# Kernel optimization log

Hardware: AMD Instinct MI355X
Metric: run time of the kernel (lower is better)

## Reference

```python
import jax, jax.numpy as jnp
import numpy as np

N_NODES = 50000
N_EDGES = 800000
D_FEAT = 128
HIDDEN = 256
N_CLASSES = 2


def setup_inputs() -> dict:
    key = jax.random.key(0)
    ks = jax.random.split(key, 9)
    x = jax.random.normal(ks[0], (N_NODES, D_FEAT), dtype=jnp.float32)
    edge_index = jax.random.randint(ks[1], (2, N_EDGES), 0, N_NODES, dtype=jnp.int32)
    # SAGEConv params: lin_l (applied to aggregated neighbors), lin_r (root), bias
    s1 = 1.0 / np.sqrt(D_FEAT)
    s2 = 1.0 / np.sqrt(HIDDEN)
    W1l = jax.random.normal(ks[2], (D_FEAT, HIDDEN), dtype=jnp.float32) * s1
    W1r = jax.random.normal(ks[3], (D_FEAT, HIDDEN), dtype=jnp.float32) * s1
    b1 = jax.random.normal(ks[4], (HIDDEN,), dtype=jnp.float32) * s1
    W2l = jax.random.normal(ks[5], (HIDDEN, N_CLASSES), dtype=jnp.float32) * s2
    W2r = jax.random.normal(ks[6], (HIDDEN, N_CLASSES), dtype=jnp.float32) * s2
    b2 = jax.random.normal(ks[7], (N_CLASSES,), dtype=jnp.float32) * s2
    return {"x": x, "edge_index": edge_index, "W1l": W1l, "W1r": W1r,
            "b1": b1, "W2l": W2l, "W2r": W2r, "b2": b2}


def _sage_conv(x, src, dst, Wl, Wr, b):
    # mean-aggregate neighbor features x[src] into destination nodes
    n = x.shape[0]
    agg = jax.ops.segment_sum(x[src], dst, num_segments=n)  # [N, d]
    deg = jax.ops.segment_sum(jnp.ones((src.shape[0],), x.dtype), dst,
                              num_segments=n)
    mean = agg / jnp.maximum(deg, 1.0)[:, None]
    return mean @ Wl + x @ Wr + b


def reference(x, edge_index, W1l, W1r, b1, W2l, W2r, b2):
    src, dst = edge_index[0], edge_index[1]
    h = jax.nn.relu(_sage_conv(x, src, dst, W1l, W1r, b1))
    embeddings = h  # dropout is identity in eval mode
    out = jax.nn.sigmoid(_sage_conv(embeddings, src, dst, W2l, W2r, b2))
    return out, embeddings
```

## Files before the change

kernel.cpp:

```cpp
#include <hip/hip_runtime.h>
#include <math.h>

#define N_NODES 50000
#define N_EDGES 800000
#define D_FEAT 128
#define HIDDEN 256
#define NB_SCAN 196
#define GEMM_BLOCKS 1563

#define PREP_CVT_B 512
#define PREP_WF_B 64
#define AGG_B 2048

#define NSLICE 64
#define SLICE_E 12500
#define NPART 8
#define PART_N 6250

typedef __bf16 bf16x8 __attribute__((ext_vector_type(8)));
typedef float f32x4 __attribute__((ext_vector_type(4)));

__device__ __forceinline__ unsigned f2b(float f) {
    unsigned u = __builtin_bit_cast(unsigned, f);
    return (u + 0x7fff + ((u >> 16) & 1)) >> 16;
}

__global__ __launch_bounds__(256) void prep(
    const float* __restrict__ x,
    const float* __restrict__ W1l, const float* __restrict__ W1r,
    unsigned* __restrict__ xb, unsigned short* __restrict__ Wfrag) {
    int b = blockIdx.x;
    int t = threadIdx.x;
    if (b < PREP_CVT_B) {
        for (int g = b * 256 + t; g < 800000; g += PREP_CVT_B * 256) {
            float4 v0 = *(const float4*)(x + (size_t)g * 8);
            float4 v1 = *(const float4*)(x + (size_t)g * 8 + 4);
            uint4 o;
            o.x = f2b(v0.x) | (f2b(v0.y) << 16);
            o.y = f2b(v0.z) | (f2b(v0.w) << 16);
            o.z = f2b(v1.x) | (f2b(v1.y) << 16);
            o.w = f2b(v1.z) | (f2b(v1.w) << 16);
            int d = g >> 4;
            int j = (g & 15) << 2;
            *(uint4*)(xb + (size_t)d * 64 + j) = o;
        }
    } else {
        for (int tt = (b - PREP_CVT_B) * 256 + t; tt < 65536; tt += PREP_WF_B * 256) {
            int j = tt & 7;
            int lane = (tt >> 3) & 63;
            int ks = (tt >> 9) & 7;
            int nt = tt >> 12;
            int k = ks * 32 + ((lane >> 4) << 3) + j;
            int n = (nt << 4) + (lane & 15);
            float v = (k < 128) ? W1l[k * 256 + n] : W1r[(k - 128) * 256 + n];
            Wfrag[tt] = (unsigned short)f2b(v);
        }
    }
}

__global__ __launch_bounds__(256) void hist_kernel(const int* __restrict__ dst,
                                                   unsigned* __restrict__ arr) {
    __shared__ unsigned hist[25000];
    int i = blockIdx.x;
    int t = threadIdx.x;
    for (int k = t; k < 25000; k += 256) hist[k] = 0;
    __syncthreads();
    int e0 = i * SLICE_E;
    for (int k = t; k < SLICE_E; k += 256) {
        int d = dst[e0 + k];
        atomicAdd(&hist[d >> 1], (d & 1) ? 65536u : 1u);
    }
    __syncthreads();
    for (int d = t; d < N_NODES; d += 256)
        arr[(size_t)i * N_NODES + d] = (hist[d >> 1] >> ((d & 1) << 4)) & 0xffffu;
}

__global__ void scan1(const unsigned* __restrict__ arr, int* __restrict__ cnt,
                      int* __restrict__ bsum) {
    __shared__ int tmp[256];
    int t = threadIdx.x;
    int i = blockIdx.x * 256 + t;
    int c = 0;
    if (i < N_NODES) {
        for (int k = 0; k < NSLICE; k++) c += (int)arr[(size_t)k * N_NODES + i];
        cnt[i] = c;
    }
    tmp[t] = c;
    __syncthreads();
    for (int off = 128; off > 0; off >>= 1) {
        if (t < off) tmp[t] += tmp[t + off];
        __syncthreads();
    }
    if (t == 0) bsum[blockIdx.x] = tmp[0];
}

__global__ void scanB(const int* __restrict__ cnt, const int* __restrict__ bsum,
                      int* __restrict__ rowbeg) {
    __shared__ int bs[256];
    __shared__ int tmp[256];
    int t = threadIdx.x;
    int b = blockIdx.x;
    bs[t] = (t < NB_SCAN) ? bsum[t] : 0;
    __syncthreads();
    for (int off = 1; off < 256; off <<= 1) {
        int y = (t >= off) ? bs[t - off] : 0;
        __syncthreads();
        bs[t] += y;
        __syncthreads();
    }
    int boff = (b == 0) ? 0 : bs[b - 1];
    int i = b * 256 + t;
    int v = (i < N_NODES) ? cnt[i] : 0;
    tmp[t] = v;
    __syncthreads();
    for (int off = 1; off < 256; off <<= 1) {
        int y = (t >= off) ? tmp[t - off] : 0;
        __syncthreads();
        tmp[t] += y;
        __syncthreads();
    }
    if (i < N_NODES) rowbeg[i] = tmp[t] - v + boff;
}

__global__ __launch_bounds__(256) void offs_kernel(const int* __restrict__ rowbeg,
                                                   unsigned* __restrict__ arr) {
    int d = blockIdx.x * 256 + threadIdx.x;
    if (d >= N_NODES) return;
    unsigned running = (unsigned)rowbeg[d];
#pragma unroll 4
    for (int k = 0; k < NSLICE; k++) {
        unsigned old = arr[(size_t)k * N_NODES + d];
        arr[(size_t)k * N_NODES + d] = running;
        running += old;
    }
}

__global__ __launch_bounds__(256) void scatter_kernel(
    const int* __restrict__ src, const int* __restrict__ dst,
    const unsigned* __restrict__ arr, unsigned short* __restrict__ esrc) {
    __shared__ unsigned off[PART_N];
    int g = blockIdx.x & 7;
    int i = blockIdx.x >> 3;
    int t = threadIdx.x;
    int lo = g * PART_N;
    for (int k = t; k < PART_N; k += 256)
        off[k] = arr[(size_t)i * N_NODES + lo + k];
    __syncthreads();
    int e0 = i * SLICE_E;
    for (int k = t; k < SLICE_E; k += 256) {
        int e = e0 + k;
        int d = dst[e];
        unsigned dl = (unsigned)(d - lo);
        if (dl < (unsigned)PART_N) {
            unsigned pos = atomicAdd(&off[dl], 1u);
            esrc[pos] = (unsigned short)src[e];
        }
    }
}

__global__ __launch_bounds__(256) void agg1(
    const unsigned* __restrict__ xb, unsigned* __restrict__ mb,
    const unsigned short* __restrict__ esrc,
    const int* __restrict__ rowbeg, const int* __restrict__ cnt) {
    int wid = (blockIdx.x * 256 + threadIdx.x) >> 6;
    int lane = threadIdx.x & 63;
    for (int d = wid; d < N_NODES; d += AGG_B * 4) {
        int beg = rowbeg[d];
        int c = cnt[d];
        int end = beg + c;
        float a0 = 0.0f, a1 = 0.0f;
        for (int base = beg; base < end; base += 64) {
            int m = end - base; if (m > 64) m = 64;
            int idx = base + lane;
            int e = (int)esrc[idx < end ? idx : end - 1];
            for (int j0 = 0; j0 < m; j0 += 8) {
#pragma unroll
                for (int j = 0; j < 8; j++) {
                    int ss = __shfl(e, j0 + j);
                    unsigned u = xb[(size_t)ss * 64 + lane];
                    float sc = (j0 + j < m) ? 1.0f : 0.0f;
                    a0 += sc * __builtin_bit_cast(float, u << 16);
                    a1 += sc * __builtin_bit_cast(float, u & 0xffff0000u);
                }
            }
        }
        float inv = 1.0f / fmaxf((float)c, 1.0f);
        mb[(size_t)d * 64 + lane] = f2b(a0 * inv) | (f2b(a1 * inv) << 16);
    }
}

__global__ __launch_bounds__(256) void gemm1ps(
    const unsigned* __restrict__ mb, const unsigned* __restrict__ xb,
    const unsigned short* __restrict__ Wfrag, const float* __restrict__ b1,
    const float* __restrict__ W2l, const float* __restrict__ W2r,
    const float* __restrict__ b2,
    float* __restrict__ h, float* __restrict__ p, float* __restrict__ s) {
    __shared__ unsigned A[32 * 128];
    __shared__ float ppart[32][4];

    int r0 = blockIdx.x * 32;
    int tid = threadIdx.x;
    int w = tid >> 6;
    int lane = tid & 63;
    int quad = lane >> 4;
    int l15 = lane & 15;

    if (tid < 128) ((float*)ppart)[tid] = 0.0f;

    int sr = tid >> 3;
    int c0 = tid & 7;
#pragma unroll
    for (int j = 0; j < 4; j++) {
        int c = c0 + (j << 3);
        uint4 v;
        if (c < 16) v = *(const uint4*)(mb + (size_t)(r0 + sr) * 64 + (c << 2));
        else        v = *(const uint4*)(xb + (size_t)(r0 + sr) * 64 + ((c - 16) << 2));
        int cp = c ^ (sr & 7);
        *(uint4*)(A + sr * 128 + (cp << 2)) = v;
    }
    __syncthreads();

    f32x4 acc[8];
#pragma unroll
    for (int i = 0; i < 8; i++) acc[i] = (f32x4){0.0f, 0.0f, 0.0f, 0.0f};

    for (int ks = 0; ks < 8; ks++) {
        bf16x8 bfr[4];
#pragma unroll
        for (int nt = 0; nt < 4; nt++) {
            int ntg = (w << 2) + nt;
            uint4 raw = *(const uint4*)(Wfrag + ((((ntg << 3) + ks) << 6) + lane) * 8);
            bfr[nt] = __builtin_bit_cast(bf16x8, raw);
        }
#pragma unroll
        for (int mt = 0; mt < 2; mt++) {
            int row = (mt << 4) + l15;
            int c = (ks << 2) + quad;
            uint4 araw = *(const uint4*)(A + row * 128 + ((c ^ (row & 7)) << 2));
            bf16x8 afr = __builtin_bit_cast(bf16x8, araw);
#pragma unroll
            for (int nt = 0; nt < 4; nt++) {
                acc[(mt << 2) + nt] = __builtin_amdgcn_mfma_f32_16x16x32_bf16(
                    afr, bfr[nt], acc[(mt << 2) + nt], 0, 0, 0);
            }
        }
    }

    float w2[4][4];
#pragma unroll
    for (int nt = 0; nt < 4; nt++) {
        int col = (w << 6) + (nt << 4) + l15;
        float2 l2 = *(const float2*)(W2l + col * 2);
        float2 r2 = *(const float2*)(W2r + col * 2);
        w2[nt][0] = l2.x; w2[nt][1] = l2.y; w2[nt][2] = r2.x; w2[nt][3] = r2.y;
    }

#pragma unroll
    for (int mt = 0; mt < 2; mt++) {
        float red[4][4];
#pragma unroll
        for (int v = 0; v < 4; v++)
#pragma unroll
            for (int r = 0; r < 4; r++) red[v][r] = 0.0f;

#pragma unroll
        for (int nt = 0; nt < 4; nt++) {
            int col = (w << 6) + (nt << 4) + l15;
            float b = b1[col];
            f32x4 v = acc[(mt << 2) + nt];
#pragma unroll
            for (int r = 0; r < 4; r++) {
                float hv = v[r] + b;
                hv = hv > 0.0f ? hv : 0.0f;
                int row = r0 + (mt << 4) + (quad << 2) + r;
                if (row < N_NODES)
                    __builtin_nontemporal_store(hv, &h[(size_t)row * 256 + col]);
                red[0][r] += hv * w2[nt][0];
                red[1][r] += hv * w2[nt][1];
                red[2][r] += hv * w2[nt][2];
                red[3][r] += hv * w2[nt][3];
            }
        }
#pragma unroll
        for (int v = 0; v < 4; v++)
#pragma unroll
            for (int r = 0; r < 4; r++) {
                red[v][r] += __shfl_xor(red[v][r], 1);
                red[v][r] += __shfl_xor(red[v][r], 2);
                red[v][r] += __shfl_xor(red[v][r], 4);
                red[v][r] += __shfl_xor(red[v][r], 8);
            }
        if (l15 == 0) {
            int lrow = (mt << 4) + (quad << 2);
#pragma unroll
            for (int r = 0; r < 4; r++)
#pragma unroll
                for (int v = 0; v < 4; v++)
                    atomicAdd(&ppart[lrow + r][v], red[v][r]);
        }
    }
    __syncthreads();

    if (tid < 32) {
        int row = r0 + tid;
        if (row < N_NODES) {
            float2 pv = {ppart[tid][0], ppart[tid][1]};
            float2 sv = {ppart[tid][2] + b2[0], ppart[tid][3] + b2[1]};
            *(float2*)(p + (size_t)row * 2) = pv;
            *(float2*)(s + (size_t)row * 2) = sv;
        }
    }
}

__global__ __launch_bounds__(256) void agg2(
    const float* __restrict__ p, const float* __restrict__ s,
    const unsigned short* __restrict__ esrc,
    const int* __restrict__ rowbeg, const int* __restrict__ cnt,
    float* __restrict__ out) {
    int wid = (blockIdx.x * 256 + threadIdx.x) >> 6;
    int lane = threadIdx.x & 63;
    for (int d = wid; d < N_NODES; d += AGG_B * 4) {
        int beg = rowbeg[d];
        int c = cnt[d];
        int end = beg + c;
        float a0 = 0.0f, a1 = 0.0f;
        for (int base = beg; base < end; base += 64) {
            int idx = base + lane;
            if (idx < end) {
                int ss = (int)esrc[idx];
                float2 v = *(const float2*)(p + (size_t)ss * 2);
                a0 += v.x; a1 += v.y;
            }
        }
#pragma unroll
        for (int off = 32; off > 0; off >>= 1) {
            a0 += __shfl_down(a0, off);
            a1 += __shfl_down(a1, off);
        }
        if (lane == 0) {
            float inv = 1.0f / fmaxf((float)c, 1.0f);
            float z0 = a0 * inv + s[(size_t)d * 2 + 0];
            float z1 = a1 * inv + s[(size_t)d * 2 + 1];
            float2 o = {1.0f / (1.0f + expf(-z0)), 1.0f / (1.0f + expf(-z1))};
            *(float2*)(out + (size_t)d * 2) = o;
        }
    }
}

extern "C" void kernel_launch(void* const* d_in, const int* in_sizes, int n_in,
                              void* d_out, int out_size, void* d_ws, size_t ws_size,
                              hipStream_t stream) {
    const float* x   = (const float*)d_in[0];
    const int*   ei  = (const int*)d_in[1];
    const float* W1l = (const float*)d_in[2];
    const float* W1r = (const float*)d_in[3];
    const float* b1  = (const float*)d_in[4];
    const float* W2l = (const float*)d_in[5];
    const float* W2r = (const float*)d_in[6];
    const float* b2  = (const float*)d_in[7];

    const int* src = ei;
    const int* dst = ei + N_EDGES;

    float* out = (float*)d_out;
    float* emb = out + (size_t)N_NODES * 2;

    int* cnt    = (int*)d_ws;
    int* rowbeg = cnt + N_NODES;
    int* bsum   = rowbeg + N_NODES;
    unsigned short* esrc = (unsigned short*)(bsum + 256);
    unsigned* xb = (unsigned*)(esrc + 800064);
    unsigned* mb = xb + (size_t)50048 * 64;
    unsigned* arr = mb;
    unsigned short* Wfrag = (unsigned short*)(mb + (size_t)50048 * 64);
    float* p = (float*)(Wfrag + 65536);
    float* s = p + (size_t)N_NODES * 2;

    prep<<<PREP_CVT_B + PREP_WF_B, 256, 0, stream>>>(x, W1l, W1r, xb, Wfrag);

    hist_kernel<<<NSLICE, 256, 0, stream>>>(dst, arr);
    scan1<<<NB_SCAN, 256, 0, stream>>>(arr, cnt, bsum);
    scanB<<<NB_SCAN, 256, 0, stream>>>(cnt, bsum, rowbeg);
    offs_kernel<<<NB_SCAN, 256, 0, stream>>>(rowbeg, arr);
    scatter_kernel<<<NSLICE * NPART, 256, 0, stream>>>(src, dst, arr, esrc);

    agg1<<<AGG_B, 256, 0, stream>>>(xb, mb, esrc, rowbeg, cnt);

    gemm1ps<<<GEMM_BLOCKS, 256, 0, stream>>>(mb, xb, Wfrag, b1, W2l, W2r, b2,
                                             emb, p, s);

    agg2<<<AGG_B, 256, 0, stream>>>(p, s, esrc, rowbeg, cnt, out);
}
```

Baseline: 239.2 us.

## Vectorize agg1 gathers with 16-byte loads, fuse offs into scanB, widen hist blocks

The first-layer aggregation now has each wavefront process four neighbor rows at once. Each group of 16 lanes loads a full 256-byte bf16 row with uint4 loads, and the groups are reduced with cross-lane xor shuffles before a vectorized store. This replaces one 4-byte load per lane per neighbor. The per-slice offset computation is folded into scanB, which removes one kernel launch. The histogram kernel also uses 1024-thread blocks to speed up the LDS clear and the atomics. The cost is more registers per lane and an extra shuffle reduction in agg1.

Measured after the change: 226.4 us. 5.4% less time.

```diff
diff --git a/kernel.cpp b/kernel.cpp
--- a/kernel.cpp
+++ b/kernel.cpp
@@ -58,20 +58,20 @@
     }
 }
 
-__global__ __launch_bounds__(256) void hist_kernel(const int* __restrict__ dst,
-                                                   unsigned* __restrict__ arr) {
+__global__ __launch_bounds__(1024) void hist_kernel(const int* __restrict__ dst,
+                                                    unsigned* __restrict__ arr) {
     __shared__ unsigned hist[25000];
     int i = blockIdx.x;
     int t = threadIdx.x;
-    for (int k = t; k < 25000; k += 256) hist[k] = 0;
+    for (int k = t; k < 25000; k += 1024) hist[k] = 0;
     __syncthreads();
     int e0 = i * SLICE_E;
-    for (int k = t; k < SLICE_E; k += 256) {
+    for (int k = t; k < SLICE_E; k += 1024) {
         int d = dst[e0 + k];
         atomicAdd(&hist[d >> 1], (d & 1) ? 65536u : 1u);
     }
     __syncthreads();
-    for (int d = t; d < N_NODES; d += 256)
+    for (int d = t; d < N_NODES; d += 1024)
         arr[(size_t)i * N_NODES + d] = (hist[d >> 1] >> ((d & 1) << 4)) & 0xffffu;
 }
 
@@ -95,7 +95,7 @@
 }
 
 __global__ void scanB(const int* __restrict__ cnt, const int* __restrict__ bsum,
-                      int* __restrict__ rowbeg) {
+                      int* __restrict__ rowbeg, unsigned* __restrict__ arr) {
     __shared__ int bs[256];
     __shared__ int tmp[256];
     int t = threadIdx.x;
@@ -119,19 +119,15 @@
         tmp[t] += y;
         __syncthreads();
     }
-    if (i < N_NODES) rowbeg[i] = tmp[t] - v + boff;
-}
-
-__global__ __launch_bounds__(256) void offs_kernel(const int* __restrict__ rowbeg,
-                                                   unsigned* __restrict__ arr) {
-    int d = blockIdx.x * 256 + threadIdx.x;
-    if (d >= N_NODES) return;
-    unsigned running = (unsigned)rowbeg[d];
+    if (i < N_NODES) {
+        unsigned running = (unsigned)(tmp[t] - v + boff);
+        rowbeg[i] = (int)running;
 #pragma unroll 4
-    for (int k = 0; k < NSLICE; k++) {
-        unsigned old = arr[(size_t)k * N_NODES + d];
-        arr[(size_t)k * N_NODES + d] = running;
-        running += old;
+        for (int k = 0; k < NSLICE; k++) {
+            unsigned old = arr[(size_t)k * N_NODES + i];
+            arr[(size_t)k * N_NODES + i] = running;
+            running += old;
+        }
     }
 }
 
@@ -164,28 +160,48 @@
     const int* __restrict__ rowbeg, const int* __restrict__ cnt) {
     int wid = (blockIdx.x * 256 + threadIdx.x) >> 6;
     int lane = threadIdx.x & 63;
+    int g = lane >> 4;
+    int i = lane & 15;
     for (int d = wid; d < N_NODES; d += AGG_B * 4) {
         int beg = rowbeg[d];
         int c = cnt[d];
         int end = beg + c;
-        float a0 = 0.0f, a1 = 0.0f;
+        float acc[8];
+#pragma unroll
+        for (int f = 0; f < 8; f++) acc[f] = 0.0f;
+
         for (int base = beg; base < end; base += 64) {
             int m = end - base; if (m > 64) m = 64;
             int idx = base + lane;
             int e = (int)esrc[idx < end ? idx : end - 1];
-            for (int j0 = 0; j0 < m; j0 += 8) {
-#pragma unroll
-                for (int j = 0; j < 8; j++) {
-                    int ss = __shfl(e, j0 + j);
-                    unsigned u = xb[(size_t)ss * 64 + lane];
-                    float sc = (j0 + j < m) ? 1.0f : 0.0f;
-                    a0 += sc * __builtin_bit_cast(float, u << 16);
-                    a1 += sc * __builtin_bit_cast(float, u & 0xffff0000u);
-                }
+            for (int j0 = 0; j0 < m; j0 += 4) {
+                int ss = __shfl(e, j0 + g);
+                float sc = (j0 + g < m) ? 1.0f : 0.0f;
+                uint4 u = *(const uint4*)(xb + (size_t)ss * 64 + (i << 2));
+                acc[0] += sc * __builtin_bit_cast(float, u.x << 16);
+                acc[1] += sc * __builtin_bit_cast(float, u.x & 0xffff0000u);
+                acc[2] += sc * __builtin_bit_cast(float, u.y << 16);
+                acc[3] += sc * __builtin_bit_cast(float, u.y & 0xffff0000u);
+                acc[4] += sc * __builtin_bit_cast(float, u.z << 16);
+                acc[5] += sc * __builtin_bit_cast(float, u.z & 0xffff0000u);
+                acc[6] += sc * __builtin_bit_cast(float, u.w << 16);
+                acc[7] += sc * __builtin_bit_cast(float, u.w & 0xffff0000u);
             }
         }
-        float inv = 1.0f / fmaxf((float)c, 1.0f);
-        mb[(size_t)d * 64 + lane] = f2b(a0 * inv) | (f2b(a1 * inv) << 16);
+#pragma unroll
+        for (int f = 0; f < 8; f++) {
+            acc[f] += __shfl_xor(acc[f], 16);
+            acc[f] += __shfl_xor(acc[f], 32);
+        }
+        if (lane < 16) {
+            float inv = 1.0f / fmaxf((float)c, 1.0f);
+            uint4 o;
+            o.x = f2b(acc[0] * inv) | (f2b(acc[1] * inv) << 16);
+            o.y = f2b(acc[2] * inv) | (f2b(acc[3] * inv) << 16);
+            o.z = f2b(acc[4] * inv) | (f2b(acc[5] * inv) << 16);
+            o.w = f2b(acc[6] * inv) | (f2b(acc[7] * inv) << 16);
+            *(uint4*)(mb + (size_t)d * 64 + (i << 2)) = o;
+        }
     }
 }
 
@@ -378,10 +394,9 @@
 
     prep<<<PREP_CVT_B + PREP_WF_B, 256, 0, stream>>>(x, W1l, W1r, xb, Wfrag);
 
-    hist_kernel<<<NSLICE, 256, 0, stream>>>(dst, arr);
+    hist_kernel<<<NSLICE, 1024, 0, stream>>>(dst, arr);
     scan1<<<NB_SCAN, 256, 0, stream>>>(arr, cnt, bsum);
-    scanB<<<NB_SCAN, 256, 0, stream>>>(cnt, bsum, rowbeg);
-    offs_kernel<<<NB_SCAN, 256, 0, stream>>>(rowbeg, arr);
+    scanB<<<NB_SCAN, 256, 0, stream>>>(cnt, bsum, rowbeg, arr);
     scatter_kernel<<<NSLICE * NPART, 256, 0, stream>>>(src, dst, arr, esrc);
 
     agg1<<<AGG_B, 256, 0, stream>>>(xb, mb, esrc, rowbeg, cnt);
```
